# Kernel optimization log

Hardware: AMD Instinct MI355X
Metric: run time of the kernel (lower is better)

The kernel has to match this reference:

```python
import jax, jax.numpy as jnp
import numpy as np
from jax import lax

NS, C_IN, C_FEAT, CROP = 16, 3, 32, 256


def _conv(x, w, b):
    # 3x3 stride-1 'SAME' conv == padding=1 in torch
    y = lax.conv_general_dilated(x, w, (1, 1), 'SAME',
                                 dimension_numbers=('NCHW', 'OIHW', 'NCHW'))
    return y + b[None, :, None, None]


def _lrn(x, size=5, alpha=1e-4, beta=0.75, k=1.0):
    # PyTorch LocalResponseNorm: x / (k + alpha/size * sum_window x^2)^beta
    pad = size // 2
    sq = jnp.pad(x * x, ((0, 0), (pad, pad), (0, 0), (0, 0)))
    c = x.shape[1]
    win = sum(sq[:, i:i + c] for i in range(size))
    return x / (k + (alpha / size) * win) ** beta


def setup_inputs() -> dict:
    key = jax.random.key(0)
    ks = jax.random.split(key, 6)
    s = 0.05
    h = np.hanning(CROP).astype(np.float32)
    cos_window = jnp.asarray(np.outer(h, h))
    return {
        'z': jax.random.normal(ks[0], (NS, C_IN, CROP, CROP), jnp.float32),
        'w1': jax.random.normal(ks[1], (C_FEAT, C_IN, 3, 3), jnp.float32) * s,
        'b1': jax.random.normal(ks[2], (C_FEAT,), jnp.float32) * s,
        'w2': jax.random.normal(ks[3], (C_FEAT, C_FEAT, 3, 3), jnp.float32) * s,
        'b2': jax.random.normal(ks[4], (C_FEAT,), jnp.float32) * s,
        'cos_window': cos_window,
        'wf': jax.random.normal(ks[5], (1, C_FEAT, CROP, CROP // 2 + 1, 2), jnp.float32) * s,
    }


def reference(z, w1, b1, w2, b2, cos_window, wf):
    # feature extractor: conv -> relu -> conv -> LRN
    f = jax.nn.relu(_conv(z, w1, b1))
    f = _lrn(_conv(f, w2, b2))
    f = f * cos_window  # (ns, 32, crop, crop)
    zf = jnp.fft.rfft2(f, axes=(-2, -1))  # (ns, 32, crop, crop//2+1) complex
    # faithful to source: w_star = conj(wf), and the loop always uses w_star[0, 1]
    # (fixed channel 1) multiplied with zf[c, l], accumulated over l. wf is detached.
    wc = lax.stop_gradient(wf[0, 1, :, :, 0] - 1j * wf[0, 1, :, :, 1])
    ftrans = wc[None, None] * jnp.sum(zf, axis=1, keepdims=True)  # (ns,1,crop,crop//2+1)
    response = jnp.fft.irfft2(ftrans, s=(CROP, CROP), axes=(-2, -1))
    return response  # (ns, 1, crop, crop)
```

## Files before the change

kernel.cpp:

```cpp
#include <hip/hip_runtime.h>
#include <math.h>

#define NS   16
#define CIN  3
#define CF   32
#define CROP 256
#define KH   129

typedef _Float16 half8  __attribute__((ext_vector_type(8)));
typedef _Float16 half4v __attribute__((ext_vector_type(4)));
typedef _Float16 half2v __attribute__((ext_vector_type(2)));
typedef float    f32x4  __attribute__((ext_vector_type(4)));

#define X_OFF 0
#define Z_OFF 21504
#define LDS_BYTES 23904

__device__ __forceinline__ int xaddr(int q, int s) {
    return X_OFF + (q << 6) + ((s ^ ((q >> 1) & 3)) << 4);
}

__device__ __forceinline__ int pi_of(int co) {
    int h = co >> 3, j = co & 7;
    return (j < 4) ? (h * 4 + j) : (16 + h * 4 + j - 4);
}
__device__ __forceinline__ int cinv_of(int p) {
    int h = (p & 15) >> 2;
    int j = (p & 3) + ((p >= 16) ? 4 : 0);
    return h * 8 + j;
}

__device__ __forceinline__ void split_pair(float v0, float v1,
                                           half2v* hp, half2v* lp) {
    _Float16 h0 = (_Float16)v0, h1 = (_Float16)v1;
    *hp = (half2v){h0, h1};
    *lp = (half2v){(_Float16)(v0 - (float)h0), (_Float16)(v1 - (float)h1)};
}

__global__ __launch_bounds__(256)
void prep(const float* __restrict__ w1, const float* __restrict__ w2,
          _Float16* __restrict__ w1pk, _Float16* __restrict__ w2lin,
          _Float16* __restrict__ TAh, _Float16* __restrict__ TAl,
          _Float16* __restrict__ G1h, _Float16* __restrict__ G1l,
          _Float16* __restrict__ G2h, _Float16* __restrict__ G2l,
          _Float16* __restrict__ G3h, _Float16* __restrict__ G3l,
          _Float16* __restrict__ G4h, _Float16* __restrict__ G4l,
          _Float16* __restrict__ TCh, _Float16* __restrict__ TCl)
{
    const int bid = blockIdx.x, tid = threadIdx.x;

    if (bid >= 67) {
        int base = (bid - 67) * 4096;
        #pragma unroll
        for (int i = 0; i < 16; ++i) {
            int e = base + tid + i * 256;
            if (e < 9216) {
                int co = e / 288;
                int r  = e - co * 288;
                int ci = r / 9, k9 = r - ci * 9;
                w2lin[(k9 * 32 + pi_of(co)) * 32 + ci] = (_Float16)w2[e];
            } else if (e < 9344) {
                int t = e - 9216;
                int lane = t & 63;
                int p = (t >> 6) * 16 + (lane & 15);
                int c = cinv_of(p);
                #pragma unroll
                for (int j = 0; j < 8; ++j) {
                    int k = ((lane >> 4) << 3) + j;
                    w1pk[t * 8 + j] = (k < 27) ? (_Float16)w1[c * 27 + k]
                                               : (_Float16)0.f;
                }
            }
        }
        return;
    }

    __shared__ float cs[256], sn[256];
    {
        float s, c;
        sincosf(0.02454369260617025967f * (float)tid, &s, &c);
        cs[tid] = c; sn[tid] = s;
    }
    __syncthreads();

    if (bid < 17) {
        int base = bid * 2048 + tid;
        #pragma unroll
        for (int i = 0; i < 8; ++i) {
            int p = base + i * 256;
            int j0 = (p & 3) * 2, lane = (p >> 2) & 63, q = p >> 8;
            int nt = q % 17, ks = q / 17;
            int x0 = ks * 32 + ((lane >> 4) << 3) + j0;
            int c = nt * 16 + (lane & 15);
            float v0 = 0.f, v1 = 0.f;
            if (c <= 128) {
                v0 =  cs[(x0 * c) & 255];
                v1 =  cs[((x0 + 1) * c) & 255];
            } else if (c >= 136 && c <= 264) {
                int cc = c - 136;
                v0 = -sn[(x0 * cc) & 255];
                v1 = -sn[((x0 + 1) * cc) & 255];
            }
            half2v hv, lv; split_pair(v0, v1, &hv, &lv);
            ((half2v*)TAh)[p] = hv; ((half2v*)TAl)[p] = lv;
        }
    } else if (bid < 49) {
        int base = (bid - 17) * 2048 + tid;
        #pragma unroll
        for (int i = 0; i < 8; ++i) {
            int p = base + i * 256;
            int j0 = (p & 3) * 2, lane = (p >> 2) & 63, q = p >> 8;
            int nt = q & 15, ks = q >> 4;
            int kk0 = ks * 32 + ((lane >> 4) << 3) + j0;
            int m  = nt * 16 + (lane & 15);
            int part = kk0 >> 8;
            int y0 = kk0 & 255;
            int i0 = (y0 * m) & 255, i1 = ((y0 + 1) * m) & 255;
            float cv0 = cs[i0], s0 = sn[i0], cv1 = cs[i1], s1 = sn[i1];
            half2v hv, lv;
            float a0 = part ? s0 : cv0,  a1 = part ? s1 : cv1;
            split_pair(a0, a1, &hv, &lv);
            ((half2v*)G1h)[p] = hv; ((half2v*)G1l)[p] = lv;
            a0 = part ? cv0 : -s0;  a1 = part ? cv1 : -s1;
            split_pair(a0, a1, &hv, &lv);
            ((half2v*)G2h)[p] = hv; ((half2v*)G2l)[p] = lv;
            a0 = (part ? -s0 : cv0) * (1.f/256.f);
            a1 = (part ? -s1 : cv1) * (1.f/256.f);
            split_pair(a0, a1, &hv, &lv);
            ((half2v*)G3h)[p] = hv; ((half2v*)G3l)[p] = lv;
            a0 = (part ? cv0 : s0) * (1.f/256.f);
            a1 = (part ? cv1 : s1) * (1.f/256.f);
            split_pair(a0, a1, &hv, &lv);
            ((half2v*)G4h)[p] = hv; ((half2v*)G4l)[p] = lv;
        }
    } else {
        int base = (bid - 49) * 2048 + tid;
        #pragma unroll
        for (int i = 0; i < 8; ++i) {
            int p = base + i * 256;
            int j0 = (p & 3) * 2, lane = (p >> 2) & 63, q = p >> 8;
            int nt = q & 15, ks = q >> 4;
            int kk0 = ks * 32 + ((lane >> 4) << 3) + j0;
            int x  = nt * 16 + (lane & 15);
            int part = (kk0 >= 144) ? 1 : 0;
            int k0 = kk0 - part * 144;
            float v0 = 0.f, v1 = 0.f;
            if (k0 <= 128) {
                float w0 = (k0 == 0 || k0 == 128) ? 1.f : 2.f;
                int ii = (k0 * x) & 255;
                v0 = (part ? -w0 * sn[ii] : w0 * cs[ii]) * (1.f/256.f);
            }
            int k1 = k0 + 1;
            if (k1 <= 128) {
                float w1w = (k1 == 0 || k1 == 128) ? 1.f : 2.f;
                int ii = (k1 * x) & 255;
                v1 = (part ? -w1w * sn[ii] : w1w * cs[ii]) * (1.f/256.f);
            }
            half2v hv, lv; split_pair(v0, v1, &hv, &lv);
            ((half2v*)TCh)[p] = hv; ((half2v*)TCl)[p] = lv;
        }
    }
}

__global__ __launch_bounds__(256, 5)
void fused_features(const float* __restrict__ z,
                    const _Float16* __restrict__ w1pk,
                    const float* __restrict__ b1,
                    const _Float16* __restrict__ w2lin,
                    const float* __restrict__ b2,
                    const float* __restrict__ cosw,
                    _Float16* __restrict__ g2h, _Float16* __restrict__ g2l)
{
    __shared__ __align__(16) unsigned char smem[LDS_BYTES];
    _Float16* ztile = (_Float16*)(smem + Z_OFF);

    const int tid  = threadIdx.x;
    const int lane = tid & 63;
    const int wv   = tid >> 6;
    const int l15  = lane & 15;
    const int lhi  = lane >> 4;

    const int n  = blockIdx.z;
    const int bx = blockIdx.x, by = blockIdx.y;
    const int fy0 = by * 16 - 1;
    const int fx0 = bx * 16 - 1;

    const int zy0 = by * 16 - 2;
    const int zx0 = bx * 16 - 2;
    for (int idx = tid; idx < CIN * 400; idx += 256) {
        int ci = idx / 400;
        int r  = idx - ci * 400;
        int yy = r / 20, xx = r - yy * 20;
        int gy = zy0 + yy, gx = zx0 + xx;
        float v = 0.0f;
        if ((unsigned)gy < CROP && (unsigned)gx < CROP)
            v = z[((n * CIN + ci) * CROP + gy) * CROP + gx];
        ztile[idx] = (_Float16)v;
    }

    half8 w1f0 = *(const half8*)(w1pk + lane * 8);
    half8 w1f1 = *(const half8*)(w1pk + 512 + lane * 8);
    float bias1v[2][4], bias2v[2][4];
    #pragma unroll
    for (int cg = 0; cg < 2; ++cg)
        #pragma unroll
        for (int r = 0; r < 4; ++r) {
            bias1v[cg][r] = b1[8 * lhi + 4 * cg + r];
            bias2v[cg][r] = b2[8 * lhi + 4 * cg + r];
        }

    int offs[8];
    #pragma unroll
    for (int j = 0; j < 8; ++j) {
        int k = lhi * 8 + j;
        int ci = k / 9, rr = k - ci * 9;
        int ky = rr / 3, kx = rr - ky * 3;
        offs[j] = (k < 27) ? (ci * 400 + ky * 20 + kx) : 0;
    }
    __syncthreads();

    const f32x4 zero4 = {0.f, 0.f, 0.f, 0.f};
    for (int t = wv; t < 21; t += 4) {
        int qp = t * 16 + l15;
        int qpc = qp < 324 ? qp : 323;
        int y = qpc / 18, x = qpc - y * 18;
        const _Float16* zb = ztile + y * 20 + x;
        half8 bfrag;
        #pragma unroll
        for (int j = 0; j < 8; ++j) bfrag[j] = zb[offs[j]];
        f32x4 d0 = __builtin_amdgcn_mfma_f32_16x16x32_f16(w1f0, bfrag, zero4, 0, 0, 0);
        f32x4 d1 = __builtin_amdgcn_mfma_f32_16x16x32_f16(w1f1, bfrag, zero4, 0, 0, 0);
        int gy = fy0 + y, gx = fx0 + x;
        bool ok = ((unsigned)gy < CROP) && ((unsigned)gx < CROP) && (qp < 324);
        half8 o8;
        #pragma unroll
        for (int r = 0; r < 4; ++r) {
            float v0 = ok ? fmaxf(d0[r] + bias1v[0][r], 0.f) : 0.f;
            float v1 = ok ? fmaxf(d1[r] + bias1v[1][r], 0.f) : 0.f;
            o8[r]     = (_Float16)v0;
            o8[4 + r] = (_Float16)v1;
        }
        *(half8*)(smem + xaddr(qp, lhi)) = o8;
    }
    __syncthreads();

    f32x4 acc[4][2];
    #pragma unroll
    for (int tt = 0; tt < 4; ++tt)
        #pragma unroll
        for (int cg = 0; cg < 2; ++cg)
            #pragma unroll
            for (int r = 0; r < 4; ++r)
                acc[tt][cg][r] = bias2v[cg][r];

    #pragma unroll
    for (int k9 = 0; k9 < 9; ++k9) {
        const int ky = k9 / 3, kx = k9 - 3 * ky;
        half8 af0 = *(const half8*)(w2lin + (k9 * 32 + l15)      * 32 + lhi * 8);
        half8 af1 = *(const half8*)(w2lin + (k9 * 32 + l15 + 16) * 32 + lhi * 8);
        #pragma unroll
        for (int tt = 0; tt < 4; ++tt) {
            int q = (wv * 4 + tt + ky) * 18 + l15 + kx;
            half8 bf = *(const half8*)(smem + xaddr(q, lhi));
            acc[tt][0] = __builtin_amdgcn_mfma_f32_16x16x32_f16(af0, bf, acc[tt][0], 0, 0, 0);
            acc[tt][1] = __builtin_amdgcn_mfma_f32_16x16x32_f16(af1, bf, acc[tt][1], 0, 0, 0);
        }
    }

    const bool bot = (lhi == 0), top = (lhi == 3);
    #pragma unroll
    for (int tt = 0; tt < 4; ++tt) {
        float aA0 = acc[tt][0][0], aA1 = acc[tt][0][1],
              aA2 = acc[tt][0][2], aA3 = acc[tt][0][3];
        float aB0 = acc[tt][1][0], aB1 = acc[tt][1][1],
              aB2 = acc[tt][1][2], aB3 = acc[tt][1][3];
        float sA0 = aA0 * aA0, sA1 = aA1 * aA1, sA2 = aA2 * aA2, sA3 = aA3 * aA3;
        float sB0 = aB0 * aB0, sB1 = aB1 * aB1, sB2 = aB2 * aB2, sB3 = aB3 * aB3;
        int up = (lane + 16) & 63, dn = (lane + 48) & 63;
        float em2 = __shfl(sB2, dn); em2 = bot ? 0.f : em2;
        float em1 = __shfl(sB3, dn); em1 = bot ? 0.f : em1;
        float ep8 = __shfl(sA0, up); ep8 = top ? 0.f : ep8;
        float ep9 = __shfl(sA1, up); ep9 = top ? 0.f : ep9;
        float s = 0.f, win = em2 + em1 + sA0 + sA1 + sA2;
        float t2, f;
        t2 = 2e-5f * win; f = fmaf(t2, fmaf(t2, 0.65625f, -0.75f), 1.0f);
        s = fmaf(aA0, f, s);  win += sA3 - em2;
        t2 = 2e-5f * win; f = fmaf(t2, fmaf(t2, 0.65625f, -0.75f), 1.0f);
        s = fmaf(aA1, f, s);  win += sB0 - em1;
        t2 = 2e-5f * win; f = fmaf(t2, fmaf(t2, 0.65625f, -0.75f), 1.0f);
        s = fmaf(aA2, f, s);  win += sB1 - sA0;
        t2 = 2e-5f * win; f = fmaf(t2, fmaf(t2, 0.65625f, -0.75f), 1.0f);
        s = fmaf(aA3, f, s);  win += sB2 - sA1;
        t2 = 2e-5f * win; f = fmaf(t2, fmaf(t2, 0.65625f, -0.75f), 1.0f);
        s = fmaf(aB0, f, s);  win += sB3 - sA2;
        t2 = 2e-5f * win; f = fmaf(t2, fmaf(t2, 0.65625f, -0.75f), 1.0f);
        s = fmaf(aB1, f, s);  win += ep8 - sA3;
        t2 = 2e-5f * win; f = fmaf(t2, fmaf(t2, 0.65625f, -0.75f), 1.0f);
        s = fmaf(aB2, f, s);  win += ep9 - sB0;
        t2 = 2e-5f * win; f = fmaf(t2, fmaf(t2, 0.65625f, -0.75f), 1.0f);
        s = fmaf(aB3, f, s);
        s += __shfl_xor(s, 16);
        s += __shfl_xor(s, 32);
        if (lhi == 0) {
            int gy = by * 16 + wv * 4 + tt, gx = bx * 16 + l15;
            float val = s * cosw[gy * CROP + gx];
            _Float16 h = (_Float16)val;
            int o = (n * CROP + gy) * CROP + gx;
            g2h[o] = h;
            g2l[o] = (_Float16)(val - (float)h);
        }
    }
}

__global__ __launch_bounds__(256, 4)
void fft_rows(const _Float16* __restrict__ g2h, const _Float16* __restrict__ g2l,
              const _Float16* __restrict__ TAh, const _Float16* __restrict__ TAl,
              _Float16* __restrict__ Zth, _Float16* __restrict__ Ztl)
{
    const int lane = threadIdx.x & 63;
    const int wu = blockIdx.x * 4 + (threadIdx.x >> 6);
    const int mt2 = wu / 17, nt = wu - mt2 * 17;
    const int l15 = lane & 15, lhi = lane >> 4;

    f32x4 a[2][3] = {};
    #pragma unroll
    for (int ks = 0; ks < 8; ++ks) {
        const int bo = ((ks * 17 + nt) * 64 + lane) * 8;
        half8 Bh = *(const half8*)(TAh + bo);
        half8 Bl = *(const half8*)(TAl + bo);
        #pragma unroll
        for (int rt = 0; rt < 2; ++rt) {
            const int ao = (mt2 * 32 + rt * 16 + l15) * 256 + ks * 32 + lhi * 8;
            half8 Ah = *(const half8*)(g2h + ao);
            half8 Al = *(const half8*)(g2l + ao);
            a[rt][0] = __builtin_amdgcn_mfma_f32_16x16x32_f16(Ah, Bh, a[rt][0], 0, 0, 0);
            a[rt][1] = __builtin_amdgcn_mfma_f32_16x16x32_f16(Ah, Bl, a[rt][1], 0, 0, 0);
            a[rt][2] = __builtin_amdgcn_mfma_f32_16x16x32_f16(Al, Bh, a[rt][2], 0, 0, 0);
        }
    }
    int c = nt * 16 + l15;
    int row_k = -1, koff = 0;
    if (c <= 128)                  { row_k = c;       koff = 0;   }
    else if (c >= 136 && c <= 264) { row_k = c - 136; koff = 256; }
    if (row_k >= 0) {
        #pragma unroll
        for (int rt = 0; rt < 2; ++rt) {
            const int rowD = mt2 * 32 + rt * 16 + lhi * 4;
            const int n = rowD >> 8, y = rowD & 255;
            half4v hv, lv;
            #pragma unroll
            for (int r = 0; r < 4; ++r) {
                float v = a[rt][0][r] + a[rt][1][r] + a[rt][2][r];
                _Float16 h = (_Float16)v;
                hv[r] = h; lv[r] = (_Float16)(v - (float)h);
            }
            size_t o = (size_t)(n * 144 + row_k) * 512 + koff + y;
            *(half4v*)(Zth + o) = hv;
            *(half4v*)(Ztl + o) = lv;
        }
    }
}

__global__ __launch_bounds__(256, 2)
void fft_cols_mul(const _Float16* __restrict__ Zth, const _Float16* __restrict__ Ztl,
                  const _Float16* __restrict__ G1h, const _Float16* __restrict__ G1l,
                  const _Float16* __restrict__ G2h, const _Float16* __restrict__ G2l,
                  const float* __restrict__ wf,
                  _Float16* __restrict__ Ph, _Float16* __restrict__ Pl)
{
    const int lane = threadIdx.x & 63;
    const int wu = blockIdx.x * 4 + (threadIdx.x >> 6);
    const int mt2 = wu >> 4, nt = wu & 15;
    const int l15 = lane & 15, lhi = lane >> 4;

    f32x4 rr[2][3] = {}, ii[2][3] = {};
    #pragma unroll
    for (int ks = 0; ks < 16; ++ks) {
        const int bo = ((ks * 16 + nt) * 64 + lane) * 8;
        half8 B1h = *(const half8*)(G1h + bo);
        half8 B1l = *(const half8*)(G1l + bo);
        half8 B2h = *(const half8*)(G2h + bo);
        half8 B2l = *(const half8*)(G2l + bo);
        #pragma unroll
        for (int rt = 0; rt < 2; ++rt) {
            const int ao = (mt2 * 32 + rt * 16 + l15) * 512 + ks * 32 + lhi * 8;
            half8 Ah = *(const half8*)(Zth + ao);
            half8 Al = *(const half8*)(Ztl + ao);
            rr[rt][0] = __builtin_amdgcn_mfma_f32_16x16x32_f16(Ah, B1h, rr[rt][0], 0, 0, 0);
            rr[rt][1] = __builtin_amdgcn_mfma_f32_16x16x32_f16(Ah, B1l, rr[rt][1], 0, 0, 0);
            rr[rt][2] = __builtin_amdgcn_mfma_f32_16x16x32_f16(Al, B1h, rr[rt][2], 0, 0, 0);
            ii[rt][0] = __builtin_amdgcn_mfma_f32_16x16x32_f16(Ah, B2h, ii[rt][0], 0, 0, 0);
            ii[rt][1] = __builtin_amdgcn_mfma_f32_16x16x32_f16(Ah, B2l, ii[rt][1], 0, 0, 0);
            ii[rt][2] = __builtin_amdgcn_mfma_f32_16x16x32_f16(Al, B2h, ii[rt][2], 0, 0, 0);
        }
    }
    const int m = nt * 16 + l15;
    const float* wf1 = wf + 256 * 129 * 2;
    #pragma unroll
    for (int rt = 0; rt < 2; ++rt) {
        const int mtr = mt2 * 2 + rt;
        const int kbase = (mtr % 9) * 16 + lhi * 4;
        const int rowP0 = mtr * 16 + lhi * 4;
        #pragma unroll
        for (int r = 0; r < 4; ++r) {
            int k = kbase + r;
            float wr = wf1[(m * 129 + k) * 2 + 0];
            float wi = wf1[(m * 129 + k) * 2 + 1];
            float fr = rr[rt][0][r] + rr[rt][1][r] + rr[rt][2][r];
            float fi = ii[rt][0][r] + ii[rt][1][r] + ii[rt][2][r];
            float pr = wr * fr + wi * fi;
            float pi = wr * fi - wi * fr;
            size_t o = (size_t)(rowP0 + r) * 512 + m;
            _Float16 h;
            h = (_Float16)pr; Ph[o] = h;       Pl[o] = (_Float16)(pr - (float)h);
            h = (_Float16)pi; Ph[o + 256] = h; Pl[o + 256] = (_Float16)(pi - (float)h);
        }
    }
}

__global__ __launch_bounds__(256, 2)
void fft_cols_inv(const _Float16* __restrict__ Ph, const _Float16* __restrict__ Pl,
                  const _Float16* __restrict__ G3h, const _Float16* __restrict__ G3l,
                  const _Float16* __restrict__ G4h, const _Float16* __restrict__ G4l,
                  _Float16* __restrict__ Bth, _Float16* __restrict__ Btl)
{
    const int lane = threadIdx.x & 63;
    const int wu = blockIdx.x * 4 + (threadIdx.x >> 6);
    const int mt2 = wu >> 4, nt = wu & 15;
    const int l15 = lane & 15, lhi = lane >> 4;

    f32x4 rr[2][3] = {}, ii[2][3] = {};
    #pragma unroll
    for (int ks = 0; ks < 16; ++ks) {
        const int bo = ((ks * 16 + nt) * 64 + lane) * 8;
        half8 B3h = *(const half8*)(G3h + bo);
        half8 B3l = *(const half8*)(G3l + bo);
        half8 B4h = *(const half8*)(G4h + bo);
        half8 B4l = *(const half8*)(G4l + bo);
        #pragma unroll
        for (int rt = 0; rt < 2; ++rt) {
            const int ao = (mt2 * 32 + rt * 16 + l15) * 512 + ks * 32 + lhi * 8;
            half8 Ah = *(const half8*)(Ph + ao);
            half8 Al = *(const half8*)(Pl + ao);
            rr[rt][0] = __builtin_amdgcn_mfma_f32_16x16x32_f16(Ah, B3h, rr[rt][0], 0, 0, 0);
            rr[rt][1] = __builtin_amdgcn_mfma_f32_16x16x32_f16(Ah, B3l, rr[rt][1], 0, 0, 0);
            rr[rt][2] = __builtin_amdgcn_mfma_f32_16x16x32_f16(Al, B3h, rr[rt][2], 0, 0, 0);
            ii[rt][0] = __builtin_amdgcn_mfma_f32_16x16x32_f16(Ah, B4h, ii[rt][0], 0, 0, 0);
            ii[rt][1] = __builtin_amdgcn_mfma_f32_16x16x32_f16(Ah, B4l, ii[rt][1], 0, 0, 0);
            ii[rt][2] = __builtin_amdgcn_mfma_f32_16x16x32_f16(Al, B4h, ii[rt][2], 0, 0, 0);
        }
    }
    const int y = nt * 16 + l15;
    #pragma unroll
    for (int rt = 0; rt < 2; ++rt) {
        const int mtr = mt2 * 2 + rt;
        const int n = mtr / 9;
        const int kbase = (mtr % 9) * 16 + lhi * 4;
        size_t base = (size_t)(n * 256 + y) * 288 + kbase;
        half4v hv0, lv0, hv1, lv1;
        #pragma unroll
        for (int r = 0; r < 4; ++r) {
            float v = rr[rt][0][r] + rr[rt][1][r] + rr[rt][2][r];
            _Float16 h = (_Float16)v;
            hv0[r] = h; lv0[r] = (_Float16)(v - (float)h);
            float v2 = ii[rt][0][r] + ii[rt][1][r] + ii[rt][2][r];
            _Float16 h2 = (_Float16)v2;
            hv1[r] = h2; lv1[r] = (_Float16)(v2 - (float)h2);
        }
        *(half4v*)(Bth + base) = hv0;
        *(half4v*)(Btl + base) = lv0;
        *(half4v*)(Bth + base + 144) = hv1;
        *(half4v*)(Btl + base + 144) = lv1;
    }
}

__global__ __launch_bounds__(256, 4)
void irfft_rows(const _Float16* __restrict__ Bth, const _Float16* __restrict__ Btl,
                const _Float16* __restrict__ TCh, const _Float16* __restrict__ TCl,
                float* __restrict__ out)
{
    const int lane = threadIdx.x & 63;
    const int wu = blockIdx.x * 4 + (threadIdx.x >> 6);
    const int mt2 = wu >> 4, nt = wu & 15;
    const int l15 = lane & 15, lhi = lane >> 4;

    f32x4 a[2][3] = {};
    #pragma unroll
    for (int ks = 0; ks < 9; ++ks) {
        const int bo = ((ks * 16 + nt) * 64 + lane) * 8;
        half8 Bh = *(const half8*)(TCh + bo);
        half8 Bl = *(const half8*)(TCl + bo);
        #pragma unroll
        for (int rt = 0; rt < 2; ++rt) {
            const int ao = (mt2 * 32 + rt * 16 + l15) * 288 + ks * 32 + lhi * 8;
            half8 Ah = *(const half8*)(Bth + ao);
            half8 Al = *(const half8*)(Btl + ao);
            a[rt][0] = __builtin_amdgcn_mfma_f32_16x16x32_f16(Ah, Bh, a[rt][0], 0, 0, 0);
            a[rt][1] = __builtin_amdgcn_mfma_f32_16x16x32_f16(Ah, Bl, a[rt][1], 0, 0, 0);
            a[rt][2] = __builtin_amdgcn_mfma_f32_16x16x32_f16(Al, Bh, a[rt][2], 0, 0, 0);
        }
    }
    const int x = nt * 16 + l15;
    #pragma unroll
    for (int rt = 0; rt < 2; ++rt) {
        const int rowD = mt2 * 32 + rt * 16 + lhi * 4;
        #pragma unroll
        for (int r = 0; r < 4; ++r)
            out[(size_t)(rowD + r) * 256 + x] = a[rt][0][r] + a[rt][1][r] + a[rt][2][r];
    }
}

extern "C" void kernel_launch(void* const* d_in, const int* in_sizes, int n_in,
                              void* d_out, int out_size, void* d_ws, size_t ws_size,
                              hipStream_t stream)
{
    const float* z    = (const float*)d_in[0];
    const float* w1   = (const float*)d_in[1];
    const float* b1   = (const float*)d_in[2];
    const float* w2   = (const float*)d_in[3];
    const float* b2   = (const float*)d_in[4];
    const float* cosw = (const float*)d_in[5];
    const float* wf   = (const float*)d_in[6];
    float* out = (float*)d_out;

    char* p = (char*)d_ws;
    auto take = [&](size_t bytes) {
        char* r = p; p += (bytes + 255) & ~(size_t)255; return r;
    };
    _Float16* g2h = (_Float16*)take(4096 * 256 * 2);
    _Float16* g2l = (_Float16*)take(4096 * 256 * 2);
    _Float16* Zth = (_Float16*)take(2304 * 512 * 2);
    _Float16* Ztl = (_Float16*)take(2304 * 512 * 2);
    _Float16* Ph  = (_Float16*)take(2304 * 512 * 2);
    _Float16* Pl  = (_Float16*)take(2304 * 512 * 2);
    _Float16* TAh = (_Float16*)take(69632 * 2);
    _Float16* TAl = (_Float16*)take(69632 * 2);
    _Float16* G1h = (_Float16*)take(131072 * 2);
    _Float16* G1l = (_Float16*)take(131072 * 2);
    _Float16* G2h = (_Float16*)take(131072 * 2);
    _Float16* G2l = (_Float16*)take(131072 * 2);
    _Float16* G3h = (_Float16*)take(131072 * 2);
    _Float16* G3l = (_Float16*)take(131072 * 2);
    _Float16* G4h = (_Float16*)take(131072 * 2);
    _Float16* G4l = (_Float16*)take(131072 * 2);
    _Float16* TCh = (_Float16*)take(73728 * 2);
    _Float16* TCl = (_Float16*)take(73728 * 2);
    _Float16* w1pk  = (_Float16*)take(1024 * 2);
    _Float16* w2lin = (_Float16*)take(9216 * 2);
    _Float16* Bth = Zth;
    _Float16* Btl = Ztl;

    prep<<<70, 256, 0, stream>>>(w1, w2, w1pk, w2lin, TAh, TAl,
                                 G1h, G1l, G2h, G2l, G3h, G3l, G4h, G4l, TCh, TCl);
    fused_features<<<dim3(16, 16, NS), 256, 0, stream>>>(z, w1pk, b1, w2lin, b2,
                                                         cosw, g2h, g2l);
    fft_rows<<<544, 256, 0, stream>>>(g2h, g2l, TAh, TAl, Zth, Ztl);
    fft_cols_mul<<<288, 256, 0, stream>>>(Zth, Ztl, G1h, G1l, G2h, G2l, wf, Ph, Pl);
    fft_cols_inv<<<288, 256, 0, stream>>>(Ph, Pl, G3h, G3l, G4h, G4l, Bth, Btl);
    irfft_rows<<<512, 256, 0, stream>>>(Bth, Btl, TCh, TCl, out);
}
```

Baseline: 119.9 us.

## Use DFT matrix symmetry to drop G2/G4, shrink GEMM tiles, enlarge feature tiles

```diff
diff --git a/kernel.cpp b/kernel.cpp
--- a/kernel.cpp
+++ b/kernel.cpp
@@ -11,10 +11,17 @@
 typedef _Float16 half4v __attribute__((ext_vector_type(4)));
 typedef _Float16 half2v __attribute__((ext_vector_type(2)));
 typedef float    f32x4  __attribute__((ext_vector_type(4)));
+typedef unsigned int u32x4 __attribute__((ext_vector_type(4)));
+
+__device__ __forceinline__ half8 neg8(half8 v) {
+    u32x4 u = __builtin_bit_cast(u32x4, v);
+    u ^= (u32x4){0x80008000u, 0x80008000u, 0x80008000u, 0x80008000u};
+    return __builtin_bit_cast(half8, u);
+}
 
 #define X_OFF 0
-#define Z_OFF 21504
-#define LDS_BYTES 23904
+#define Z_OFF 39936
+#define LDS_BYTES 44256
 
 __device__ __forceinline__ int xaddr(int q, int s) {
     return X_OFF + (q << 6) + ((s ^ ((q >> 1) & 3)) << 4);
@@ -42,9 +49,7 @@
           _Float16* __restrict__ w1pk, _Float16* __restrict__ w2lin,
           _Float16* __restrict__ TAh, _Float16* __restrict__ TAl,
           _Float16* __restrict__ G1h, _Float16* __restrict__ G1l,
-          _Float16* __restrict__ G2h, _Float16* __restrict__ G2l,
           _Float16* __restrict__ G3h, _Float16* __restrict__ G3l,
-          _Float16* __restrict__ G4h, _Float16* __restrict__ G4l,
           _Float16* __restrict__ TCh, _Float16* __restrict__ TCl)
 {
     const int bid = blockIdx.x, tid = threadIdx.x;
@@ -121,17 +126,10 @@
             float a0 = part ? s0 : cv0,  a1 = part ? s1 : cv1;
             split_pair(a0, a1, &hv, &lv);
             ((half2v*)G1h)[p] = hv; ((half2v*)G1l)[p] = lv;
-            a0 = part ? cv0 : -s0;  a1 = part ? cv1 : -s1;
-            split_pair(a0, a1, &hv, &lv);
-            ((half2v*)G2h)[p] = hv; ((half2v*)G2l)[p] = lv;
             a0 = (part ? -s0 : cv0) * (1.f/256.f);
             a1 = (part ? -s1 : cv1) * (1.f/256.f);
             split_pair(a0, a1, &hv, &lv);
             ((half2v*)G3h)[p] = hv; ((half2v*)G3l)[p] = lv;
-            a0 = (part ? cv0 : s0) * (1.f/256.f);
-            a1 = (part ? cv1 : s1) * (1.f/256.f);
-            split_pair(a0, a1, &hv, &lv);
-            ((half2v*)G4h)[p] = hv; ((half2v*)G4l)[p] = lv;
         }
     } else {
         int base = (bid - 49) * 2048 + tid;
@@ -162,7 +160,7 @@
     }
 }
 
-__global__ __launch_bounds__(256, 5)
+__global__ __launch_bounds__(512, 6)
 void fused_features(const float* __restrict__ z,
                     const _Float16* __restrict__ w1pk,
                     const float* __restrict__ b1,
@@ -182,14 +180,14 @@
 
     const int n  = blockIdx.z;
     const int bx = blockIdx.x, by = blockIdx.y;
-    const int fy0 = by * 16 - 1;
+    const int fy0 = by * 32 - 1;
     const int fx0 = bx * 16 - 1;
 
-    const int zy0 = by * 16 - 2;
+    const int zy0 = by * 32 - 2;
     const int zx0 = bx * 16 - 2;
-    for (int idx = tid; idx < CIN * 400; idx += 256) {
-        int ci = idx / 400;
-        int r  = idx - ci * 400;
+    for (int idx = tid; idx < CIN * 720; idx += 512) {
+        int ci = idx / 720;
+        int r  = idx - ci * 720;
         int yy = r / 20, xx = r - yy * 20;
         int gy = zy0 + yy, gx = zx0 + xx;
         float v = 0.0f;
@@ -215,14 +213,14 @@
         int k = lhi * 8 + j;
         int ci = k / 9, rr = k - ci * 9;
         int ky = rr / 3, kx = rr - ky * 3;
-        offs[j] = (k < 27) ? (ci * 400 + ky * 20 + kx) : 0;
+        offs[j] = (k < 27) ? (ci * 720 + ky * 20 + kx) : 0;
     }
     __syncthreads();
 
     const f32x4 zero4 = {0.f, 0.f, 0.f, 0.f};
-    for (int t = wv; t < 21; t += 4) {
+    for (int t = wv; t < 39; t += 8) {
         int qp = t * 16 + l15;
-        int qpc = qp < 324 ? qp : 323;
+        int qpc = qp < 612 ? qp : 611;
         int y = qpc / 18, x = qpc - y * 18;
         const _Float16* zb = ztile + y * 20 + x;
         half8 bfrag;
@@ -231,7 +229,7 @@
         f32x4 d0 = __builtin_amdgcn_mfma_f32_16x16x32_f16(w1f0, bfrag, zero4, 0, 0, 0);
         f32x4 d1 = __builtin_amdgcn_mfma_f32_16x16x32_f16(w1f1, bfrag, zero4, 0, 0, 0);
         int gy = fy0 + y, gx = fx0 + x;
-        bool ok = ((unsigned)gy < CROP) && ((unsigned)gx < CROP) && (qp < 324);
+        bool ok = ((unsigned)gy < CROP) && ((unsigned)gx < CROP) && (qp < 612);
         half8 o8;
         #pragma unroll
         for (int r = 0; r < 4; ++r) {
@@ -302,7 +300,7 @@
         s += __shfl_xor(s, 16);
         s += __shfl_xor(s, 32);
         if (lhi == 0) {
-            int gy = by * 16 + wv * 4 + tt, gx = bx * 16 + l15;
+            int gy = by * 32 + wv * 4 + tt, gx = bx * 16 + l15;
             float val = s * cosw[gy * CROP + gx];
             _Float16 h = (_Float16)val;
             int o = (n * CROP + gy) * CROP + gx;
@@ -319,159 +317,162 @@
 {
     const int lane = threadIdx.x & 63;
     const int wu = blockIdx.x * 4 + (threadIdx.x >> 6);
-    const int mt2 = wu / 17, nt = wu - mt2 * 17;
+    const int mt = wu / 17, nt = wu - mt * 17;
     const int l15 = lane & 15, lhi = lane >> 4;
-
-    f32x4 a[2][3] = {};
+    const int rowA = mt * 16 + l15;
+
+    f32x4 a0 = {}, a1 = {}, a2 = {};
     #pragma unroll
     for (int ks = 0; ks < 8; ++ks) {
+        const int ao = rowA * 256 + ks * 32 + lhi * 8;
+        half8 Ah = *(const half8*)(g2h + ao);
+        half8 Al = *(const half8*)(g2l + ao);
         const int bo = ((ks * 17 + nt) * 64 + lane) * 8;
         half8 Bh = *(const half8*)(TAh + bo);
         half8 Bl = *(const half8*)(TAl + bo);
-        #pragma unroll
-        for (int rt = 0; rt < 2; ++rt) {
-            const int ao = (mt2 * 32 + rt * 16 + l15) * 256 + ks * 32 + lhi * 8;
-            half8 Ah = *(const half8*)(g2h + ao);
-            half8 Al = *(const half8*)(g2l + ao);
-            a[rt][0] = __builtin_amdgcn_mfma_f32_16x16x32_f16(Ah, Bh, a[rt][0], 0, 0, 0);
-            a[rt][1] = __builtin_amdgcn_mfma_f32_16x16x32_f16(Ah, Bl, a[rt][1], 0, 0, 0);
-            a[rt][2] = __builtin_amdgcn_mfma_f32_16x16x32_f16(Al, Bh, a[rt][2], 0, 0, 0);
-        }
-    }
+        a0 = __builtin_amdgcn_mfma_f32_16x16x32_f16(Ah, Bh, a0, 0, 0, 0);
+        a1 = __builtin_amdgcn_mfma_f32_16x16x32_f16(Ah, Bl, a1, 0, 0, 0);
+        a2 = __builtin_amdgcn_mfma_f32_16x16x32_f16(Al, Bh, a2, 0, 0, 0);
+    }
+    f32x4 acc;
+    #pragma unroll
+    for (int r = 0; r < 4; ++r) acc[r] = a0[r] + a1[r] + a2[r];
+
+    const int rowD = mt * 16 + lhi * 4;
+    const int n = rowD >> 8, y = rowD & 255;
     int c = nt * 16 + l15;
     int row_k = -1, koff = 0;
     if (c <= 128)                  { row_k = c;       koff = 0;   }
     else if (c >= 136 && c <= 264) { row_k = c - 136; koff = 256; }
     if (row_k >= 0) {
-        #pragma unroll
-        for (int rt = 0; rt < 2; ++rt) {
-            const int rowD = mt2 * 32 + rt * 16 + lhi * 4;
-            const int n = rowD >> 8, y = rowD & 255;
-            half4v hv, lv;
-            #pragma unroll
-            for (int r = 0; r < 4; ++r) {
-                float v = a[rt][0][r] + a[rt][1][r] + a[rt][2][r];
-                _Float16 h = (_Float16)v;
-                hv[r] = h; lv[r] = (_Float16)(v - (float)h);
-            }
-            size_t o = (size_t)(n * 144 + row_k) * 512 + koff + y;
-            *(half4v*)(Zth + o) = hv;
-            *(half4v*)(Ztl + o) = lv;
-        }
+        half4v hv, lv;
+        #pragma unroll
+        for (int r = 0; r < 4; ++r) {
+            float v = acc[r];
+            _Float16 h = (_Float16)v;
+            hv[r] = h; lv[r] = (_Float16)(v - (float)h);
+        }
+        size_t o = (size_t)(n * 144 + row_k) * 512 + koff + y;
+        *(half4v*)(Zth + o) = hv;
+        *(half4v*)(Ztl + o) = lv;
     }
 }
 
 __global__ __launch_bounds__(256, 2)
 void fft_cols_mul(const _Float16* __restrict__ Zth, const _Float16* __restrict__ Ztl,
                   const _Float16* __restrict__ G1h, const _Float16* __restrict__ G1l,
-                  const _Float16* __restrict__ G2h, const _Float16* __restrict__ G2l,
                   const float* __restrict__ wf,
                   _Float16* __restrict__ Ph, _Float16* __restrict__ Pl)
 {
     const int lane = threadIdx.x & 63;
     const int wu = blockIdx.x * 4 + (threadIdx.x >> 6);
-    const int mt2 = wu >> 4, nt = wu & 15;
+    const int mt = wu >> 4, nt = wu & 15;
     const int l15 = lane & 15, lhi = lane >> 4;
-
-    f32x4 rr[2][3] = {}, ii[2][3] = {};
-    #pragma unroll
-    for (int ks = 0; ks < 16; ++ks) {
-        const int bo = ((ks * 16 + nt) * 64 + lane) * 8;
-        half8 B1h = *(const half8*)(G1h + bo);
-        half8 B1l = *(const half8*)(G1l + bo);
-        half8 B2h = *(const half8*)(G2h + bo);
-        half8 B2l = *(const half8*)(G2l + bo);
-        #pragma unroll
-        for (int rt = 0; rt < 2; ++rt) {
-            const int ao = (mt2 * 32 + rt * 16 + l15) * 512 + ks * 32 + lhi * 8;
-            half8 Ah = *(const half8*)(Zth + ao);
-            half8 Al = *(const half8*)(Ztl + ao);
-            rr[rt][0] = __builtin_amdgcn_mfma_f32_16x16x32_f16(Ah, B1h, rr[rt][0], 0, 0, 0);
-            rr[rt][1] = __builtin_amdgcn_mfma_f32_16x16x32_f16(Ah, B1l, rr[rt][1], 0, 0, 0);
-            rr[rt][2] = __builtin_amdgcn_mfma_f32_16x16x32_f16(Al, B1h, rr[rt][2], 0, 0, 0);
-            ii[rt][0] = __builtin_amdgcn_mfma_f32_16x16x32_f16(Ah, B2h, ii[rt][0], 0, 0, 0);
-            ii[rt][1] = __builtin_amdgcn_mfma_f32_16x16x32_f16(Ah, B2l, ii[rt][1], 0, 0, 0);
-            ii[rt][2] = __builtin_amdgcn_mfma_f32_16x16x32_f16(Al, B2h, ii[rt][2], 0, 0, 0);
-        }
-    }
+    const int rowA = mt * 16 + l15;
+
+    f32x4 r0 = {}, r1 = {}, r2 = {}, i0 = {}, i1 = {}, i2 = {};
+    #pragma unroll
+    for (int ks = 0; ks < 8; ++ks) {
+        const int ao0 = rowA * 512 + ks * 32 + lhi * 8;
+        half8 Ah0 = *(const half8*)(Zth + ao0);
+        half8 Al0 = *(const half8*)(Ztl + ao0);
+        half8 Ah1 = *(const half8*)(Zth + ao0 + 256);
+        half8 Al1 = *(const half8*)(Ztl + ao0 + 256);
+        const int bo0 = ((ks * 16 + nt) * 64 + lane) * 8;
+        half8 B0h = *(const half8*)(G1h + bo0);
+        half8 B0l = *(const half8*)(G1l + bo0);
+        half8 B1h_ = *(const half8*)(G1h + bo0 + 65536);
+        half8 B1l_ = *(const half8*)(G1l + bo0 + 65536);
+        half8 nB1h = neg8(B1h_), nB1l = neg8(B1l_);
+        r0 = __builtin_amdgcn_mfma_f32_16x16x32_f16(Ah0, B0h,  r0, 0, 0, 0);
+        r1 = __builtin_amdgcn_mfma_f32_16x16x32_f16(Ah0, B0l,  r1, 0, 0, 0);
+        r2 = __builtin_amdgcn_mfma_f32_16x16x32_f16(Al0, B0h,  r2, 0, 0, 0);
+        r0 = __builtin_amdgcn_mfma_f32_16x16x32_f16(Ah1, B1h_, r0, 0, 0, 0);
+        r1 = __builtin_amdgcn_mfma_f32_16x16x32_f16(Ah1, B1l_, r1, 0, 0, 0);
+        r2 = __builtin_amdgcn_mfma_f32_16x16x32_f16(Al1, B1h_, r2, 0, 0, 0);
+        i0 = __builtin_amdgcn_mfma_f32_16x16x32_f16(Ah0, nB1h, i0, 0, 0, 0);
+        i1 = __builtin_amdgcn_mfma_f32_16x16x32_f16(Ah0, nB1l, i1, 0, 0, 0);
+        i2 = __builtin_amdgcn_mfma_f32_16x16x32_f16(Al0, nB1h, i2, 0, 0, 0);
+        i0 = __builtin_amdgcn_mfma_f32_16x16x32_f16(Ah1, B0h,  i0, 0, 0, 0);
+        i1 = __builtin_amdgcn_mfma_f32_16x16x32_f16(Ah1, B0l,  i1, 0, 0, 0);
+        i2 = __builtin_amdgcn_mfma_f32_16x16x32_f16(Al1, B0h,  i2, 0, 0, 0);
+    }
+    const int kbase = (mt % 9) * 16 + lhi * 4;
+    const int rowP0 = mt * 16 + lhi * 4;
     const int m = nt * 16 + l15;
     const float* wf1 = wf + 256 * 129 * 2;
     #pragma unroll
-    for (int rt = 0; rt < 2; ++rt) {
-        const int mtr = mt2 * 2 + rt;
-        const int kbase = (mtr % 9) * 16 + lhi * 4;
-        const int rowP0 = mtr * 16 + lhi * 4;
-        #pragma unroll
-        for (int r = 0; r < 4; ++r) {
-            int k = kbase + r;
-            float wr = wf1[(m * 129 + k) * 2 + 0];
-            float wi = wf1[(m * 129 + k) * 2 + 1];
-            float fr = rr[rt][0][r] + rr[rt][1][r] + rr[rt][2][r];
-            float fi = ii[rt][0][r] + ii[rt][1][r] + ii[rt][2][r];
-            float pr = wr * fr + wi * fi;
-            float pi = wr * fi - wi * fr;
-            size_t o = (size_t)(rowP0 + r) * 512 + m;
-            _Float16 h;
-            h = (_Float16)pr; Ph[o] = h;       Pl[o] = (_Float16)(pr - (float)h);
-            h = (_Float16)pi; Ph[o + 256] = h; Pl[o + 256] = (_Float16)(pi - (float)h);
-        }
+    for (int r = 0; r < 4; ++r) {
+        int k = kbase + r;
+        float wr = wf1[(m * 129 + k) * 2 + 0];
+        float wi = wf1[(m * 129 + k) * 2 + 1];
+        float fr = r0[r] + r1[r] + r2[r];
+        float fi = i0[r] + i1[r] + i2[r];
+        float pr = wr * fr + wi * fi;
+        float pi = wr * fi - wi * fr;
+        size_t o = (size_t)(rowP0 + r) * 512 + m;
+        _Float16 h;
+        h = (_Float16)pr; Ph[o] = h;       Pl[o] = (_Float16)(pr - (float)h);
+        h = (_Float16)pi; Ph[o + 256] = h; Pl[o + 256] = (_Float16)(pi - (float)h);
     }
 }
 
 __global__ __launch_bounds__(256, 2)
 void fft_cols_inv(const _Float16* __restrict__ Ph, const _Float16* __restrict__ Pl,
                   const _Float16* __restrict__ G3h, const _Float16* __restrict__ G3l,
-                  const _Float16* __restrict__ G4h, const _Float16* __restrict__ G4l,
                   _Float16* __restrict__ Bth, _Float16* __restrict__ Btl)
 {
     const int lane = threadIdx.x & 63;
     const int wu = blockIdx.x * 4 + (threadIdx.x >> 6);
-    const int mt2 = wu >> 4, nt = wu & 15;
+    const int mt = wu >> 4, nt = wu & 15;
     const int l15 = lane & 15, lhi = lane >> 4;
-
-    f32x4 rr[2][3] = {}, ii[2][3] = {};
-    #pragma unroll
-    for (int ks = 0; ks < 16; ++ks) {
-        const int bo = ((ks * 16 + nt) * 64 + lane) * 8;
-        half8 B3h = *(const half8*)(G3h + bo);
-        half8 B3l = *(const half8*)(G3l + bo);
-        half8 B4h = *(const half8*)(G4h + bo);
-        half8 B4l = *(const half8*)(G4l + bo);
-        #pragma unroll
-        for (int rt = 0; rt < 2; ++rt) {
-            const int ao = (mt2 * 32 + rt * 16 + l15) * 512 + ks * 32 + lhi * 8;
-            half8 Ah = *(const half8*)(Ph + ao);
-            half8 Al = *(const half8*)(Pl + ao);
-            rr[rt][0] = __builtin_amdgcn_mfma_f32_16x16x32_f16(Ah, B3h, rr[rt][0], 0, 0, 0);
-            rr[rt][1] = __builtin_amdgcn_mfma_f32_16x16x32_f16(Ah, B3l, rr[rt][1], 0, 0, 0);
-            rr[rt][2] = __builtin_amdgcn_mfma_f32_16x16x32_f16(Al, B3h, rr[rt][2], 0, 0, 0);
-            ii[rt][0] = __builtin_amdgcn_mfma_f32_16x16x32_f16(Ah, B4h, ii[rt][0], 0, 0, 0);
-            ii[rt][1] = __builtin_amdgcn_mfma_f32_16x16x32_f16(Ah, B4l, ii[rt][1], 0, 0, 0);
-            ii[rt][2] = __builtin_amdgcn_mfma_f32_16x16x32_f16(Al, B4h, ii[rt][2], 0, 0, 0);
-        }
-    }
+    const int rowA = mt * 16 + l15;
+
+    f32x4 r0 = {}, r1 = {}, r2 = {}, i0 = {}, i1 = {}, i2 = {};
+    #pragma unroll
+    for (int ks = 0; ks < 8; ++ks) {
+        const int ao0 = rowA * 512 + ks * 32 + lhi * 8;
+        half8 Ah0 = *(const half8*)(Ph + ao0);
+        half8 Al0 = *(const half8*)(Pl + ao0);
+        half8 Ah1 = *(const half8*)(Ph + ao0 + 256);
+        half8 Al1 = *(const half8*)(Pl + ao0 + 256);
+        const int bo0 = ((ks * 16 + nt) * 64 + lane) * 8;
+        half8 B0h = *(const half8*)(G3h + bo0);
+        half8 B0l = *(const half8*)(G3l + bo0);
+        half8 B1h_ = *(const half8*)(G3h + bo0 + 65536);
+        half8 B1l_ = *(const half8*)(G3l + bo0 + 65536);
+        half8 nB1h = neg8(B1h_), nB1l = neg8(B1l_);
+        r0 = __builtin_amdgcn_mfma_f32_16x16x32_f16(Ah0, B0h,  r0, 0, 0, 0);
+        r1 = __builtin_amdgcn_mfma_f32_16x16x32_f16(Ah0, B0l,  r1, 0, 0, 0);
+        r2 = __builtin_amdgcn_mfma_f32_16x16x32_f16(Al0, B0h,  r2, 0, 0, 0);
+        r0 = __builtin_amdgcn_mfma_f32_16x16x32_f16(Ah1, B1h_, r0, 0, 0, 0);
+        r1 = __builtin_amdgcn_mfma_f32_16x16x32_f16(Ah1, B1l_, r1, 0, 0, 0);
+        r2 = __builtin_amdgcn_mfma_f32_16x16x32_f16(Al1, B1h_, r2, 0, 0, 0);
+        i0 = __builtin_amdgcn_mfma_f32_16x16x32_f16(Ah0, nB1h, i0, 0, 0, 0);
+        i1 = __builtin_amdgcn_mfma_f32_16x16x32_f16(Ah0, nB1l, i1, 0, 0, 0);
+        i2 = __builtin_amdgcn_mfma_f32_16x16x32_f16(Al0, nB1h, i2, 0, 0, 0);
+        i0 = __builtin_amdgcn_mfma_f32_16x16x32_f16(Ah1, B0h,  i0, 0, 0, 0);
+        i1 = __builtin_amdgcn_mfma_f32_16x16x32_f16(Ah1, B0l,  i1, 0, 0, 0);
+        i2 = __builtin_amdgcn_mfma_f32_16x16x32_f16(Al1, B0h,  i2, 0, 0, 0);
+    }
+    const int n = mt / 9;
+    const int kbase = (mt % 9) * 16 + lhi * 4;
     const int y = nt * 16 + l15;
-    #pragma unroll
-    for (int rt = 0; rt < 2; ++rt) {
-        const int mtr = mt2 * 2 + rt;
-        const int n = mtr / 9;
-        const int kbase = (mtr % 9) * 16 + lhi * 4;
-        size_t base = (size_t)(n * 256 + y) * 288 + kbase;
-        half4v hv0, lv0, hv1, lv1;
-        #pragma unroll
-        for (int r = 0; r < 4; ++r) {
-            float v = rr[rt][0][r] + rr[rt][1][r] + rr[rt][2][r];
-            _Float16 h = (_Float16)v;
-            hv0[r] = h; lv0[r] = (_Float16)(v - (float)h);
-            float v2 = ii[rt][0][r] + ii[rt][1][r] + ii[rt][2][r];
-            _Float16 h2 = (_Float16)v2;
-            hv1[r] = h2; lv1[r] = (_Float16)(v2 - (float)h2);
-        }
-        *(half4v*)(Bth + base) = hv0;
-        *(half4v*)(Btl + base) = lv0;
-        *(half4v*)(Bth + base + 144) = hv1;
-        *(half4v*)(Btl + base + 144) = lv1;
-    }
+    size_t base = (size_t)(n * 256 + y) * 288 + kbase;
+    half4v hv0, lv0, hv1, lv1;
+    #pragma unroll
+    for (int r = 0; r < 4; ++r) {
+        float v = r0[r] + r1[r] + r2[r];
+        _Float16 h = (_Float16)v;
+        hv0[r] = h; lv0[r] = (_Float16)(v - (float)h);
+        float v2 = i0[r] + i1[r] + i2[r];
+        _Float16 h2 = (_Float16)v2;
+        hv1[r] = h2; lv1[r] = (_Float16)(v2 - (float)h2);
+    }
+    *(half4v*)(Bth + base) = hv0;
+    *(half4v*)(Btl + base) = lv0;
+    *(half4v*)(Bth + base + 144) = hv1;
+    *(half4v*)(Btl + base + 144) = lv1;
 }
 
 __global__ __launch_bounds__(256, 4)
@@ -481,33 +482,28 @@
 {
     const int lane = threadIdx.x & 63;
     const int wu = blockIdx.x * 4 + (threadIdx.x >> 6);
-    const int mt2 = wu >> 4, nt = wu & 15;
+    const int mt = wu >> 4, nt = wu & 15;
     const int l15 = lane & 15, lhi = lane >> 4;
-
-    f32x4 a[2][3] = {};
+    const int rowA = mt * 16 + l15;
+
+    f32x4 a0 = {}, a1 = {}, a2 = {};
     #pragma unroll
     for (int ks = 0; ks < 9; ++ks) {
+        const int ao = rowA * 288 + ks * 32 + lhi * 8;
+        half8 Ah = *(const half8*)(Bth + ao);
+        half8 Al = *(const half8*)(Btl + ao);
         const int bo = ((ks * 16 + nt) * 64 + lane) * 8;
         half8 Bh = *(const half8*)(TCh + bo);
         half8 Bl = *(const half8*)(TCl + bo);
-        #pragma unroll
-        for (int rt = 0; rt < 2; ++rt) {
-            const int ao = (mt2 * 32 + rt * 16 + l15) * 288 + ks * 32 + lhi * 8;
-            half8 Ah = *(const half8*)(Bth + ao);
-            half8 Al = *(const half8*)(Btl + ao);
-            a[rt][0] = __builtin_amdgcn_mfma_f32_16x16x32_f16(Ah, Bh, a[rt][0], 0, 0, 0);
-            a[rt][1] = __builtin_amdgcn_mfma_f32_16x16x32_f16(Ah, Bl, a[rt][1], 0, 0, 0);
-            a[rt][2] = __builtin_amdgcn_mfma_f32_16x16x32_f16(Al, Bh, a[rt][2], 0, 0, 0);
-        }
-    }
+        a0 = __builtin_amdgcn_mfma_f32_16x16x32_f16(Ah, Bh, a0, 0, 0, 0);
+        a1 = __builtin_amdgcn_mfma_f32_16x16x32_f16(Ah, Bl, a1, 0, 0, 0);
+        a2 = __builtin_amdgcn_mfma_f32_16x16x32_f16(Al, Bh, a2, 0, 0, 0);
+    }
+    const int rowD = mt * 16 + lhi * 4;
     const int x = nt * 16 + l15;
     #pragma unroll
-    for (int rt = 0; rt < 2; ++rt) {
-        const int rowD = mt2 * 32 + rt * 16 + lhi * 4;
-        #pragma unroll
-        for (int r = 0; r < 4; ++r)
-            out[(size_t)(rowD + r) * 256 + x] = a[rt][0][r] + a[rt][1][r] + a[rt][2][r];
-    }
+    for (int r = 0; r < 4; ++r)
+        out[(size_t)(rowD + r) * 256 + x] = a0[r] + a1[r] + a2[r];
 }
 
 extern "C" void kernel_launch(void* const* d_in, const int* in_sizes, int n_in,
@@ -537,12 +533,8 @@
     _Float16* TAl = (_Float16*)take(69632 * 2);
     _Float16* G1h = (_Float16*)take(131072 * 2);
     _Float16* G1l = (_Float16*)take(131072 * 2);
-    _Float16* G2h = (_Float16*)take(131072 * 2);
-    _Float16* G2l = (_Float16*)take(131072 * 2);
     _Float16* G3h = (_Float16*)take(131072 * 2);
     _Float16* G3l = (_Float16*)take(131072 * 2);
-    _Float16* G4h = (_Float16*)take(131072 * 2);
-    _Float16* G4l = (_Float16*)take(131072 * 2);
     _Float16* TCh = (_Float16*)take(73728 * 2);
     _Float16* TCl = (_Float16*)take(73728 * 2);
     _Float16* w1pk  = (_Float16*)take(1024 * 2);
@@ -551,11 +543,11 @@
     _Float16* Btl = Ztl;
 
     prep<<<70, 256, 0, stream>>>(w1, w2, w1pk, w2lin, TAh, TAl,
-                                 G1h, G1l, G2h, G2l, G3h, G3l, G4h, G4l, TCh, TCl);
-    fused_features<<<dim3(16, 16, NS), 256, 0, stream>>>(z, w1pk, b1, w2lin, b2,
-                                                         cosw, g2h, g2l);
-    fft_rows<<<544, 256, 0, stream>>>(g2h, g2l, TAh, TAl, Zth, Ztl);
-    fft_cols_mul<<<288, 256, 0, stream>>>(Zth, Ztl, G1h, G1l, G2h, G2l, wf, Ph, Pl);
-    fft_cols_inv<<<288, 256, 0, stream>>>(Ph, Pl, G3h, G3l, G4h, G4l, Bth, Btl);
-    irfft_rows<<<512, 256, 0, stream>>>(Bth, Btl, TCh, TCl, out);
-}
+                                 G1h, G1l, G3h, G3l, TCh, TCl);
+    fused_features<<<dim3(16, 8, NS), 512, 0, stream>>>(z, w1pk, b1, w2lin, b2,
+                                                        cosw, g2h, g2l);
+    fft_rows<<<1088, 256, 0, stream>>>(g2h, g2l, TAh, TAl, Zth, Ztl);
+    fft_cols_mul<<<576, 256, 0, stream>>>(Zth, Ztl, G1h, G1l, wf, Ph, Pl);
+    fft_cols_inv<<<576, 256, 0, stream>>>(Ph, Pl, G3h, G3l, Bth, Btl);
+    irfft_rows<<<1024, 256, 0, stream>>>(Bth, Btl, TCh, TCl, out);
+}
```

New measurement: 143.4 us. 19.6% more time.
